# Kernel optimization log

Hardware: AMD Instinct MI355X
Metric: run time of the kernel (lower is better)

Reference implementation:

```python
import jax, jax.numpy as jnp
import numpy as np

N = 100000      # nodes
E = 1600000     # edges (avg degree 16)
IN = 128        # in_channels
H = 64          # hidden
C = 2           # num_classes
G = 256         # graphs in batch


def _glorot(key, shape):
    lim = np.sqrt(6.0 / (shape[0] + shape[1])).astype(np.float32)
    return jax.random.uniform(key, shape, jnp.float32, -lim, lim)


def setup_inputs() -> dict:
    key = jax.random.key(0)
    ks = jax.random.split(key, 8)
    x = jax.random.normal(ks[0], (N, IN), jnp.float32)
    edge_index = jax.random.randint(ks[1], (2, E), 0, N)
    batch = jnp.sort(jax.random.randint(ks[2], (N,), 0, G))
    W1 = _glorot(ks[3], (IN, H)); b1 = jnp.zeros((H,), jnp.float32)
    W2 = _glorot(ks[4], (H, H));  b2 = jnp.zeros((H,), jnp.float32)
    Wc1 = _glorot(ks[5], (H, H // 2)); bc1 = jnp.zeros((H // 2,), jnp.float32)
    Wc2 = _glorot(ks[6], (H // 2, C)); bc2 = jnp.zeros((C,), jnp.float32)
    return dict(x=x, edge_index=edge_index, batch=batch,
                W1=W1, b1=b1, W2=W2, b2=b2,
                Wc1=Wc1, bc1=bc1, Wc2=Wc2, bc2=bc2)


def gcn_conv(x, W, b, src, dst, n):
    """PyG GCNConv: linear -> symmetric-normalized scatter-add with self-loops."""
    h = x @ W                                   # [N, out]
    # degree over dst including the added self-loop (edge_weight = 1)
    deg = jax.ops.segment_sum(jnp.ones((src.shape[0],), h.dtype), dst,
                              num_segments=n) + 1.0
    dinv = jax.lax.rsqrt(deg)                   # deg^{-1/2}
    norm = dinv[src] * dinv[dst]                # [E]
    msg = norm[:, None] * h[src]                # gather + normalize
    out = jax.ops.segment_sum(msg, dst, num_segments=n)
    out = out + (dinv * dinv)[:, None] * h      # self-loop contribution
    return out + b


def reference(x, edge_index, batch, W1, b1, W2, b2, Wc1, bc1, Wc2, bc2):
    src, dst = edge_index[0], edge_index[1]
    h = jax.nn.relu(gcn_conv(x, W1, b1, src, dst, N))
    h = jax.nn.relu(gcn_conv(h, W2, b2, src, dst, N))
    # global mean pool over graph ids
    s = jax.ops.segment_sum(h, batch, num_segments=G)
    cnt = jax.ops.segment_sum(jnp.ones((N,), h.dtype), batch, num_segments=G)
    g = s / jnp.maximum(cnt, 1.0)[:, None]      # [G, H]
    return jax.nn.relu(g @ Wc1 + bc1) @ Wc2 + bc2  # [G, C]
```

## Files before the change

### kernel.cpp

```cpp
#include <hip/hip_runtime.h>

#define N_NODES 100000
#define N_EDGES 1600000
#define IN_CH   128
#define HID     64
#define NG      256
#define CAP     64
#define NXCD    8
#define XRANGE  ((N_NODES + NXCD - 1) / NXCD)

typedef __attribute__((ext_vector_type(8))) short bf16x8;
typedef __attribute__((ext_vector_type(4))) float f32x4;

__device__ __forceinline__ unsigned short f2bf(float f) {
    union { float f; unsigned u; } v; v.f = f;
    unsigned r = v.u + 0x7FFF + ((v.u >> 16) & 1);
    return (unsigned short)(r >> 16);
}
__device__ __forceinline__ float bfval(unsigned short h) {
    return __uint_as_float((unsigned)h << 16);
}
__device__ __forceinline__ unsigned int f2bf2(float lo, float hi) {
    return (unsigned int)f2bf(lo) | ((unsigned int)f2bf(hi) << 16);
}
__device__ __forceinline__ float bf_lo(unsigned int p) { return __uint_as_float(p << 16); }
__device__ __forceinline__ float bf_hi(unsigned int p) { return __uint_as_float(p & 0xFFFF0000u); }

__global__ void k_zero(int* __restrict__ p, int n4) {
    int i = blockIdx.x * blockDim.x + threadIdx.x;
    if (i < n4) reinterpret_cast<int4*>(p)[i] = (int4){0, 0, 0, 0};
}

__global__ void k_fillx(const int* __restrict__ src, const int* __restrict__ dst,
                        int* __restrict__ fillpos, int* __restrict__ col) {
    const int xcd = blockIdx.x & (NXCD - 1);
    const int chunk = blockIdx.x >> 3;
    const int nchunks = gridDim.x >> 3;
    const int lo = xcd * XRANGE;
    const int hi = (lo + XRANGE < N_NODES) ? lo + XRANGE : N_NODES;
    const int per = (N_EDGES + nchunks - 1) / nchunks;
    const int e0 = chunk * per;
    const int e1 = (e0 + per < N_EDGES) ? e0 + per : N_EDGES;
    for (int e = e0 + threadIdx.x; e < e1; e += blockDim.x) {
        int d = dst[e];
        if (d < lo || d >= hi) continue;
        int p = atomicAdd(&fillpos[d], 1);
        if (p < CAP) col[(long)d * CAP + p] = src[e];
    }
}

__global__ void k_prep(const int* __restrict__ deg, float* __restrict__ dinv,
                       int* __restrict__ col, const int* __restrict__ batch,
                       int* __restrict__ start) {
    int i = blockIdx.x * blockDim.x + threadIdx.x;
    if (i >= N_NODES) return;
    int n = deg[i];
    dinv[i] = rsqrtf((float)n + 1.0f);
    n = n < CAP ? n : CAP;
    int n16 = (n + 15) & ~15;
    int* crow = col + (long)i * CAP;
    for (int p = n; p < n16; ++p) crow[p] = i;
    int b = batch[i];
    int prev = (i == 0) ? -1 : batch[i - 1];
    for (int g = prev + 1; g <= b; ++g) start[g] = i;
    if (i == N_NODES - 1)
        for (int g = b + 1; g <= NG; ++g) start[g] = N_NODES;
}

__global__ void k_wcvt(const float* __restrict__ W1, const float* __restrict__ W2,
                       unsigned short* __restrict__ W1hi, unsigned short* __restrict__ W1lo,
                       unsigned short* __restrict__ W2hi, unsigned short* __restrict__ W2lo) {
    int t = blockIdx.x * blockDim.x + threadIdx.x;
    if (t < 64 * IN_CH) {
        int e = t & 7, lane = (t >> 3) & 63, q = t >> 9;
        int kk = q >> 2, cb = q & 3, kg = lane >> 4, r = lane & 15;
        float v = W1[(kk * 32 + kg * 8 + e) * 64 + cb * 16 + r];
        unsigned short hh = f2bf(v);
        W1hi[t] = hh;
        W1lo[t] = f2bf(v - bfval(hh));
    } else if (t < 64 * IN_CH + 64 * HID) {
        int t2 = t - 64 * IN_CH;
        int e = t2 & 7, lane = (t2 >> 3) & 63, q = t2 >> 9;
        int kk = q >> 2, cb = q & 3, kg = lane >> 4, r = lane & 15;
        float v = W2[(kk * 32 + kg * 8 + e) * 64 + cb * 16 + r];
        unsigned short hh = f2bf(v);
        W2hi[t2] = hh;
        W2lo[t2] = f2bf(v - bfval(hh));
    }
}

template <int K>
__global__ void __launch_bounds__(256) k_linear(const float* __restrict__ x,
                                                const unsigned short* __restrict__ Whi,
                                                const unsigned short* __restrict__ Wlo,
                                                const float* __restrict__ dinv,
                                                unsigned short* __restrict__ hs) {
    __shared__ f32x4 red[2][64][8];
    const int tid  = threadIdx.x;
    const int wv   = tid >> 6;
    const int pair = wv >> 1;
    const int h    = wv & 1;
    const int lane = tid & 63;
    const int row16 = lane & 15;
    const int kg    = lane >> 4;
    const int n0 = (blockIdx.x * 2 + pair) * 32;
    const bool valid = (n0 < N_NODES);

    f32x4 acc[2][4];
#pragma unroll
    for (int bt = 0; bt < 2; ++bt)
#pragma unroll
        for (int cb = 0; cb < 4; ++cb) acc[bt][cb] = (f32x4){0.f, 0.f, 0.f, 0.f};

    const int NKK = K / 32;
    const int kkBeg = h * (NKK / 2);
    const int kkEnd = kkBeg + NKK / 2;

#pragma unroll
    for (int kk = kkBeg; kk < kkEnd; ++kk) {
        bf16x8 xhi0, xlo0, xhi1, xlo1;
        {
            int rr = n0 + row16;
            rr = rr < N_NODES ? rr : N_NODES - 1;
            const float* ap = x + (long)rr * K + kk * 32 + kg * 8;
            float4 b0 = *reinterpret_cast<const float4*>(ap);
            float4 b1 = *reinterpret_cast<const float4*>(ap + 4);
#define CVT(dsthi, dstlo, i, val) { unsigned short h_ = f2bf(val); dsthi[i] = (short)h_; \
                                    dstlo[i] = (short)f2bf((val) - bfval(h_)); }
            CVT(xhi0, xlo0, 0, b0.x) CVT(xhi0, xlo0, 1, b0.y)
            CVT(xhi0, xlo0, 2, b0.z) CVT(xhi0, xlo0, 3, b0.w)
            CVT(xhi0, xlo0, 4, b1.x) CVT(xhi0, xlo0, 5, b1.y)
            CVT(xhi0, xlo0, 6, b1.z) CVT(xhi0, xlo0, 7, b1.w)
        }
        {
            int rr = n0 + 16 + row16;
            rr = rr < N_NODES ? rr : N_NODES - 1;
            const float* ap = x + (long)rr * K + kk * 32 + kg * 8;
            float4 b0 = *reinterpret_cast<const float4*>(ap);
            float4 b1 = *reinterpret_cast<const float4*>(ap + 4);
            CVT(xhi1, xlo1, 0, b0.x) CVT(xhi1, xlo1, 1, b0.y)
            CVT(xhi1, xlo1, 2, b0.z) CVT(xhi1, xlo1, 3, b0.w)
            CVT(xhi1, xlo1, 4, b1.x) CVT(xhi1, xlo1, 5, b1.y)
            CVT(xhi1, xlo1, 6, b1.z) CVT(xhi1, xlo1, 7, b1.w)
#undef CVT
        }
#pragma unroll
        for (int cb = 0; cb < 4; ++cb) {
            long foff = (long)((kk * 4 + cb) * 64 + lane) * 8;
            bf16x8 wh = *reinterpret_cast<const bf16x8*>(Whi + foff);
            bf16x8 wl = *reinterpret_cast<const bf16x8*>(Wlo + foff);
            acc[0][cb] = __builtin_amdgcn_mfma_f32_16x16x32_bf16(wh, xhi0, acc[0][cb], 0, 0, 0);
            acc[0][cb] = __builtin_amdgcn_mfma_f32_16x16x32_bf16(wh, xlo0, acc[0][cb], 0, 0, 0);
            acc[0][cb] = __builtin_amdgcn_mfma_f32_16x16x32_bf16(wl, xhi0, acc[0][cb], 0, 0, 0);
            acc[1][cb] = __builtin_amdgcn_mfma_f32_16x16x32_bf16(wh, xhi1, acc[1][cb], 0, 0, 0);
            acc[1][cb] = __builtin_amdgcn_mfma_f32_16x16x32_bf16(wh, xlo1, acc[1][cb], 0, 0, 0);
            acc[1][cb] = __builtin_amdgcn_mfma_f32_16x16x32_bf16(wl, xhi1, acc[1][cb], 0, 0, 0);
        }
    }

    if (h == 1) {
#pragma unroll
        for (int bt = 0; bt < 2; ++bt)
#pragma unroll
            for (int cb = 0; cb < 4; ++cb) red[pair][lane][bt * 4 + cb] = acc[bt][cb];
    }
    __syncthreads();
    if (h == 0 && valid) {
#pragma unroll
        for (int bt = 0; bt < 2; ++bt) {
            int n = n0 + bt * 16 + row16;
            float d = dinv[n];
#pragma unroll
            for (int cb = 0; cb < 4; ++cb) {
                f32x4 a = acc[bt][cb];
                f32x4 b = red[pair][lane][bt * 4 + cb];
                float v0 = (a[0] + b[0]) * d;
                float v1 = (a[1] + b[1]) * d;
                float v2 = (a[2] + b[2]) * d;
                float v3 = (a[3] + b[3]) * d;
                uint2 p;
                p.x = f2bf2(v0, v1);
                p.y = f2bf2(v2, v3);
                *reinterpret_cast<uint2*>(&hs[(long)n * 64 + cb * 16 + kg * 4]) = p;
            }
        }
    }
}

__global__ void k_gather(const int* __restrict__ deg, const int* __restrict__ col,
                         const unsigned int* __restrict__ hs2,
                         const float* __restrict__ dinv, const float* __restrict__ bias,
                         float* __restrict__ out) {
    int t = blockIdx.x * blockDim.x + threadIdx.x;
    int lane = t & 63;
    int half = lane >> 5;
    int c2 = lane & 31;
    int i = ((t >> 6) << 1) + half;
    if (i >= N_NODES) return;
    const int4* crow4 = reinterpret_cast<const int4*>(col + (long)i * CAP);
    int n = deg[i];
    n = n < CAP ? n : CAP;
    int n16 = (n + 15) & ~15;
    const unsigned int* hsc = hs2 + c2;
    unsigned int self = hsc[(long)i * 32];
    float selfL = bf_lo(self), selfH = bf_hi(self);
    float aL = selfL, aH = selfH;

    for (int e0 = 0; e0 < n16; e0 += 16) {
        int4 q0 = crow4[(e0 >> 2) + 0];
        int4 q1 = crow4[(e0 >> 2) + 1];
        int4 q2 = crow4[(e0 >> 2) + 2];
        int4 q3 = crow4[(e0 >> 2) + 3];
        unsigned int v[16];
        v[0]  = hsc[(long)q0.x * 32]; v[1]  = hsc[(long)q0.y * 32];
        v[2]  = hsc[(long)q0.z * 32]; v[3]  = hsc[(long)q0.w * 32];
        v[4]  = hsc[(long)q1.x * 32]; v[5]  = hsc[(long)q1.y * 32];
        v[6]  = hsc[(long)q1.z * 32]; v[7]  = hsc[(long)q1.w * 32];
        v[8]  = hsc[(long)q2.x * 32]; v[9]  = hsc[(long)q2.y * 32];
        v[10] = hsc[(long)q2.z * 32]; v[11] = hsc[(long)q2.w * 32];
        v[12] = hsc[(long)q3.x * 32]; v[13] = hsc[(long)q3.y * 32];
        v[14] = hsc[(long)q3.z * 32]; v[15] = hsc[(long)q3.w * 32];
#pragma unroll
        for (int j = 0; j < 16; ++j) {
            aL += bf_lo(v[j]);
            aH += bf_hi(v[j]);
        }
    }
    float fE = (float)(n16 - n);
    aL = fmaf(-fE, selfL, aL);
    aH = fmaf(-fE, selfH, aH);

    float di = dinv[i];
    float vL = fmaf(di, aL, bias[2 * c2]);
    float vH = fmaf(di, aH, bias[2 * c2 + 1]);
    float2 o;
    o.x = vL > 0.f ? vL : 0.f;
    o.y = vH > 0.f ? vH : 0.f;
    *reinterpret_cast<float2*>(&out[(long)i * 64 + 2 * c2]) = o;
}

__global__ void k_poolhead(const float* __restrict__ a, const int* __restrict__ start,
                           const float* __restrict__ Wc1, const float* __restrict__ bc1,
                           const float* __restrict__ Wc2, const float* __restrict__ bc2,
                           float* __restrict__ out) {
    __shared__ float partial[4][64];
    __shared__ float gvec[64];
    __shared__ float tvec[32];
    int g = blockIdx.x;
    int w = threadIdx.x >> 6;
    int j = threadIdx.x & 63;
    int s0 = start[g], s1 = start[g + 1];
    float acc = 0.f;
    for (int i = s0 + w; i < s1; i += 4)
        acc += a[(long)i * 64 + j];
    partial[w][j] = acc;
    __syncthreads();
    if (w == 0) {
        float c = (float)(s1 - s0);
        c = c > 1.f ? c : 1.f;
        gvec[j] = (partial[0][j] + partial[1][j] + partial[2][j] + partial[3][j]) / c;
    }
    __syncthreads();
    if (threadIdx.x < 32) {
        int jj = threadIdx.x;
        float acc2 = bc1[jj];
#pragma unroll 8
        for (int k = 0; k < 64; ++k) acc2 = fmaf(gvec[k], Wc1[k * 32 + jj], acc2);
        tvec[jj] = acc2 > 0.f ? acc2 : 0.f;
    }
    __syncthreads();
    if (threadIdx.x < 2) {
        int jj = threadIdx.x;
        float acc2 = bc2[jj];
#pragma unroll
        for (int k = 0; k < 32; ++k) acc2 = fmaf(tvec[k], Wc2[k * 2 + jj], acc2);
        out[g * 2 + jj] = acc2;
    }
}

extern "C" void kernel_launch(void* const* d_in, const int* in_sizes, int n_in,
                              void* d_out, int out_size, void* d_ws, size_t ws_size,
                              hipStream_t stream) {
    const float* x    = (const float*)d_in[0];
    const int*   ei   = (const int*)d_in[1];
    const int*   batch= (const int*)d_in[2];
    const float* W1   = (const float*)d_in[3];
    const float* b1   = (const float*)d_in[4];
    const float* W2   = (const float*)d_in[5];
    const float* b2   = (const float*)d_in[6];
    const float* Wc1  = (const float*)d_in[7];
    const float* bc1  = (const float*)d_in[8];
    const float* Wc2  = (const float*)d_in[9];
    const float* bc2  = (const float*)d_in[10];
    float* out = (float*)d_out;

    const int* src = ei;
    const int* dst = ei + N_EDGES;

    char* ws = (char*)d_ws;
    size_t off = 0;
    auto alloc = [&](size_t bytes) {
        void* p = ws + off;
        off += (bytes + 255) & ~(size_t)255;
        return p;
    };
    unsigned short* hs = (unsigned short*)alloc((size_t)N_NODES * HID * 2);
    float* agg     = (float*)alloc((size_t)N_NODES * HID * sizeof(float));
    int*   col     = (int*)  alloc((size_t)N_NODES * CAP * sizeof(int) + 256);
    float* dinv    = (float*)alloc(N_NODES * sizeof(float));
    int*   fillpos = (int*)  alloc((N_NODES + 4) * sizeof(int));
    int*   start   = (int*)  alloc((NG + 1) * sizeof(int));
    unsigned short* W1hi = (unsigned short*)alloc(64 * IN_CH * 2);
    unsigned short* W1lo = (unsigned short*)alloc(64 * IN_CH * 2);
    unsigned short* W2hi = (unsigned short*)alloc(64 * HID * 2);
    unsigned short* W2lo = (unsigned short*)alloc(64 * HID * 2);

    const int TB = 256;

    k_wcvt<<<(64 * (IN_CH + HID) + TB - 1) / TB, TB, 0, stream>>>(W1, W2, W1hi, W1lo, W2hi, W2lo);

    {
        const int nz4 = (N_NODES + 3) / 4;
        k_zero<<<(nz4 + TB - 1) / TB, TB, 0, stream>>>(fillpos, nz4);
        k_fillx<<<2048, TB, 0, stream>>>(src, dst, fillpos, col);
        k_prep<<<(N_NODES + TB - 1) / TB, TB, 0, stream>>>(fillpos, dinv, col, batch, start);
    }

    const int gatherBlocks = ((N_NODES + 1) / 2 * 64 + TB - 1) / TB;
    const int linBlocks = (N_NODES + 63) / 64;

    k_linear<IN_CH><<<linBlocks, 256, 0, stream>>>(x, W1hi, W1lo, dinv, hs);
    k_gather<<<gatherBlocks, TB, 0, stream>>>(fillpos, col, (const unsigned int*)hs, dinv, b1, agg);

    k_linear<HID><<<linBlocks, 256, 0, stream>>>(agg, W2hi, W2lo, dinv, hs);
    k_gather<<<gatherBlocks, TB, 0, stream>>>(fillpos, col, (const unsigned int*)hs, dinv, b2, agg);

    k_poolhead<<<NG, 256, 0, stream>>>(agg, start, Wc1, bc1, Wc2, bc2, out);
}
```

Baseline: 212.9 us.

## Co-schedule first linear layer with CSR fill in one fused launch

```diff
diff --git a/kernel.cpp b/kernel.cpp
--- a/kernel.cpp
+++ b/kernel.cpp
@@ -8,6 +8,8 @@
 #define CAP     64
 #define NXCD    8
 #define XRANGE  ((N_NODES + NXCD - 1) / NXCD)
+#define FILLB   2048
+#define LINB    ((N_NODES + 63) / 64)
 
 typedef __attribute__((ext_vector_type(8))) short bf16x8;
 typedef __attribute__((ext_vector_type(4))) float f32x4;
@@ -26,51 +28,12 @@
 __device__ __forceinline__ float bf_lo(unsigned int p) { return __uint_as_float(p << 16); }
 __device__ __forceinline__ float bf_hi(unsigned int p) { return __uint_as_float(p & 0xFFFF0000u); }
 
-__global__ void k_zero(int* __restrict__ p, int n4) {
-    int i = blockIdx.x * blockDim.x + threadIdx.x;
-    if (i < n4) reinterpret_cast<int4*>(p)[i] = (int4){0, 0, 0, 0};
-}
-
-__global__ void k_fillx(const int* __restrict__ src, const int* __restrict__ dst,
-                        int* __restrict__ fillpos, int* __restrict__ col) {
-    const int xcd = blockIdx.x & (NXCD - 1);
-    const int chunk = blockIdx.x >> 3;
-    const int nchunks = gridDim.x >> 3;
-    const int lo = xcd * XRANGE;
-    const int hi = (lo + XRANGE < N_NODES) ? lo + XRANGE : N_NODES;
-    const int per = (N_EDGES + nchunks - 1) / nchunks;
-    const int e0 = chunk * per;
-    const int e1 = (e0 + per < N_EDGES) ? e0 + per : N_EDGES;
-    for (int e = e0 + threadIdx.x; e < e1; e += blockDim.x) {
-        int d = dst[e];
-        if (d < lo || d >= hi) continue;
-        int p = atomicAdd(&fillpos[d], 1);
-        if (p < CAP) col[(long)d * CAP + p] = src[e];
-    }
-}
-
-__global__ void k_prep(const int* __restrict__ deg, float* __restrict__ dinv,
-                       int* __restrict__ col, const int* __restrict__ batch,
-                       int* __restrict__ start) {
-    int i = blockIdx.x * blockDim.x + threadIdx.x;
-    if (i >= N_NODES) return;
-    int n = deg[i];
-    dinv[i] = rsqrtf((float)n + 1.0f);
-    n = n < CAP ? n : CAP;
-    int n16 = (n + 15) & ~15;
-    int* crow = col + (long)i * CAP;
-    for (int p = n; p < n16; ++p) crow[p] = i;
-    int b = batch[i];
-    int prev = (i == 0) ? -1 : batch[i - 1];
-    for (int g = prev + 1; g <= b; ++g) start[g] = i;
-    if (i == N_NODES - 1)
-        for (int g = b + 1; g <= NG; ++g) start[g] = N_NODES;
-}
-
-__global__ void k_wcvt(const float* __restrict__ W1, const float* __restrict__ W2,
+__global__ void k_init(const float* __restrict__ W1, const float* __restrict__ W2,
                        unsigned short* __restrict__ W1hi, unsigned short* __restrict__ W1lo,
-                       unsigned short* __restrict__ W2hi, unsigned short* __restrict__ W2lo) {
+                       unsigned short* __restrict__ W2hi, unsigned short* __restrict__ W2lo,
+                       int* __restrict__ fillpos) {
     int t = blockIdx.x * blockDim.x + threadIdx.x;
+    if (t < N_NODES / 4) reinterpret_cast<int4*>(fillpos)[t] = (int4){0, 0, 0, 0};
     if (t < 64 * IN_CH) {
         int e = t & 7, lane = (t >> 3) & 63, q = t >> 9;
         int kk = q >> 2, cb = q & 3, kg = lane >> 4, r = lane & 15;
@@ -89,21 +52,18 @@
     }
 }
 
-template <int K>
-__global__ void __launch_bounds__(256) k_linear(const float* __restrict__ x,
-                                                const unsigned short* __restrict__ Whi,
-                                                const unsigned short* __restrict__ Wlo,
-                                                const float* __restrict__ dinv,
-                                                unsigned short* __restrict__ hs) {
-    __shared__ f32x4 red[2][64][8];
-    const int tid  = threadIdx.x;
+template <int K, bool SC>
+__device__ __forceinline__ void lin_body(int bid, int tid, const float* __restrict__ x,
+        const unsigned short* __restrict__ Whi, const unsigned short* __restrict__ Wlo,
+        const float* __restrict__ dinv, unsigned short* __restrict__ hs,
+        float* __restrict__ fout, f32x4 red[2][64][8]) {
     const int wv   = tid >> 6;
     const int pair = wv >> 1;
     const int h    = wv & 1;
     const int lane = tid & 63;
     const int row16 = lane & 15;
     const int kg    = lane >> 4;
-    const int n0 = (blockIdx.x * 2 + pair) * 32;
+    const int n0 = (bid * 2 + pair) * 32;
     const bool valid = (n0 < N_NODES);
 
     f32x4 acc[2][4];
@@ -169,25 +129,92 @@
 #pragma unroll
         for (int bt = 0; bt < 2; ++bt) {
             int n = n0 + bt * 16 + row16;
-            float d = dinv[n];
 #pragma unroll
             for (int cb = 0; cb < 4; ++cb) {
                 f32x4 a = acc[bt][cb];
                 f32x4 b = red[pair][lane][bt * 4 + cb];
-                float v0 = (a[0] + b[0]) * d;
-                float v1 = (a[1] + b[1]) * d;
-                float v2 = (a[2] + b[2]) * d;
-                float v3 = (a[3] + b[3]) * d;
-                uint2 p;
-                p.x = f2bf2(v0, v1);
-                p.y = f2bf2(v2, v3);
-                *reinterpret_cast<uint2*>(&hs[(long)n * 64 + cb * 16 + kg * 4]) = p;
+                if (SC) {
+                    float d = dinv[n];
+                    uint2 p;
+                    p.x = f2bf2((a[0] + b[0]) * d, (a[1] + b[1]) * d);
+                    p.y = f2bf2((a[2] + b[2]) * d, (a[3] + b[3]) * d);
+                    *reinterpret_cast<uint2*>(&hs[(long)n * 64 + cb * 16 + kg * 4]) = p;
+                } else {
+                    float4 st;
+                    st.x = a[0] + b[0]; st.y = a[1] + b[1];
+                    st.z = a[2] + b[2]; st.w = a[3] + b[3];
+                    *reinterpret_cast<float4*>(&fout[(long)n * 64 + cb * 16 + kg * 4]) = st;
+                }
             }
         }
     }
 }
 
-__global__ void k_gather(const int* __restrict__ deg, const int* __restrict__ col,
+__global__ void __launch_bounds__(256) k_fuse(const float* __restrict__ x,
+        const unsigned short* __restrict__ W1hi, const unsigned short* __restrict__ W1lo,
+        float* __restrict__ agg,
+        const int* __restrict__ src, const int* __restrict__ dst,
+        int* __restrict__ fillpos, int* __restrict__ col) {
+    __shared__ f32x4 red[2][64][8];
+    if (blockIdx.x < LINB) {
+        lin_body<IN_CH, false>(blockIdx.x, threadIdx.x, x, W1hi, W1lo, nullptr, nullptr, agg, red);
+    } else {
+        const int fb = blockIdx.x - LINB;
+        const int xcd = fb & (NXCD - 1);
+        const int chunk = fb >> 3;
+        const int nchunks = FILLB >> 3;
+        const int lo = xcd * XRANGE;
+        const int hi = (lo + XRANGE < N_NODES) ? lo + XRANGE : N_NODES;
+        const int per = (N_EDGES + nchunks - 1) / nchunks;
+        const int e0 = chunk * per;
+        const int e1 = (e0 + per < N_EDGES) ? e0 + per : N_EDGES;
+        for (int e = e0 + threadIdx.x; e < e1; e += blockDim.x) {
+            int d = dst[e];
+            if (d < lo || d >= hi) continue;
+            int p = atomicAdd(&fillpos[d], 1);
+            if (p < CAP) col[(long)d * CAP + p] = src[e] * 32;
+        }
+    }
+}
+
+template <int K>
+__global__ void __launch_bounds__(256) k_linear(const float* __restrict__ x,
+        const unsigned short* __restrict__ Whi, const unsigned short* __restrict__ Wlo,
+        const float* __restrict__ dinv, unsigned short* __restrict__ hs) {
+    __shared__ f32x4 red[2][64][8];
+    lin_body<K, true>(blockIdx.x, threadIdx.x, x, Whi, Wlo, dinv, hs, nullptr, red);
+}
+
+__global__ void k_prep(const int* __restrict__ fillpos, float* __restrict__ dinv,
+                       int* __restrict__ col, const int* __restrict__ batch,
+                       int* __restrict__ start) {
+    int i = blockIdx.x * blockDim.x + threadIdx.x;
+    if (i >= N_NODES) return;
+    int n = fillpos[i];
+    dinv[i] = rsqrtf((float)n + 1.0f);
+    n = n < CAP ? n : CAP;
+    int n16 = (n + 15) & ~15;
+    int* crow = col + (long)i * CAP;
+    int self32 = i * 32;
+    for (int p = n; p < n16; ++p) crow[p] = self32;
+    int b = batch[i];
+    int prev = (i == 0) ? -1 : batch[i - 1];
+    for (int g = prev + 1; g <= b; ++g) start[g] = i;
+    if (i == N_NODES - 1)
+        for (int g = b + 1; g <= NG; ++g) start[g] = N_NODES;
+}
+
+__global__ void k_scale(const float* __restrict__ fin, const float* __restrict__ dinv,
+                        unsigned int* __restrict__ hs2) {
+    int t = blockIdx.x * blockDim.x + threadIdx.x;
+    if (t >= N_NODES * 32) return;
+    int n = t >> 5;
+    float d = dinv[n];
+    float2 a = reinterpret_cast<const float2*>(fin)[t];
+    hs2[t] = f2bf2(a.x * d, a.y * d);
+}
+
+__global__ void k_gather(const int* __restrict__ fillpos, const int* __restrict__ col,
                          const unsigned int* __restrict__ hs2,
                          const float* __restrict__ dinv, const float* __restrict__ bias,
                          float* __restrict__ out) {
@@ -198,7 +225,7 @@
     int i = ((t >> 6) << 1) + half;
     if (i >= N_NODES) return;
     const int4* crow4 = reinterpret_cast<const int4*>(col + (long)i * CAP);
-    int n = deg[i];
+    int n = fillpos[i];
     n = n < CAP ? n : CAP;
     int n16 = (n + 15) & ~15;
     const unsigned int* hsc = hs2 + c2;
@@ -212,14 +239,14 @@
         int4 q2 = crow4[(e0 >> 2) + 2];
         int4 q3 = crow4[(e0 >> 2) + 3];
         unsigned int v[16];
-        v[0]  = hsc[(long)q0.x * 32]; v[1]  = hsc[(long)q0.y * 32];
-        v[2]  = hsc[(long)q0.z * 32]; v[3]  = hsc[(long)q0.w * 32];
-        v[4]  = hsc[(long)q1.x * 32]; v[5]  = hsc[(long)q1.y * 32];
-        v[6]  = hsc[(long)q1.z * 32]; v[7]  = hsc[(long)q1.w * 32];
-        v[8]  = hsc[(long)q2.x * 32]; v[9]  = hsc[(long)q2.y * 32];
-        v[10] = hsc[(long)q2.z * 32]; v[11] = hsc[(long)q2.w * 32];
-        v[12] = hsc[(long)q3.x * 32]; v[13] = hsc[(long)q3.y * 32];
-        v[14] = hsc[(long)q3.z * 32]; v[15] = hsc[(long)q3.w * 32];
+        v[0]  = hsc[(long)q0.x]; v[1]  = hsc[(long)q0.y];
+        v[2]  = hsc[(long)q0.z]; v[3]  = hsc[(long)q0.w];
+        v[4]  = hsc[(long)q1.x]; v[5]  = hsc[(long)q1.y];
+        v[6]  = hsc[(long)q1.z]; v[7]  = hsc[(long)q1.w];
+        v[8]  = hsc[(long)q2.x]; v[9]  = hsc[(long)q2.y];
+        v[10] = hsc[(long)q2.z]; v[11] = hsc[(long)q2.w];
+        v[12] = hsc[(long)q3.x]; v[13] = hsc[(long)q3.y];
+        v[14] = hsc[(long)q3.z]; v[15] = hsc[(long)q3.w];
 #pragma unroll
         for (int j = 0; j < 16; ++j) {
             aL += bf_lo(v[j]);
@@ -317,22 +344,19 @@
 
     const int TB = 256;
 
-    k_wcvt<<<(64 * (IN_CH + HID) + TB - 1) / TB, TB, 0, stream>>>(W1, W2, W1hi, W1lo, W2hi, W2lo);
-
-    {
-        const int nz4 = (N_NODES + 3) / 4;
-        k_zero<<<(nz4 + TB - 1) / TB, TB, 0, stream>>>(fillpos, nz4);
-        k_fillx<<<2048, TB, 0, stream>>>(src, dst, fillpos, col);
-        k_prep<<<(N_NODES + TB - 1) / TB, TB, 0, stream>>>(fillpos, dinv, col, batch, start);
-    }
+    k_init<<<(N_NODES / 4 + TB - 1) / TB, TB, 0, stream>>>(W1, W2, W1hi, W1lo, W2hi, W2lo, fillpos);
+
+    k_fuse<<<LINB + FILLB, TB, 0, stream>>>(x, W1hi, W1lo, agg, src, dst, fillpos, col);
+
+    k_prep<<<(N_NODES + TB - 1) / TB, TB, 0, stream>>>(fillpos, dinv, col, batch, start);
+
+    k_scale<<<(N_NODES * 32 + TB - 1) / TB, TB, 0, stream>>>(agg, dinv, (unsigned int*)hs);
 
     const int gatherBlocks = ((N_NODES + 1) / 2 * 64 + TB - 1) / TB;
-    const int linBlocks = (N_NODES + 63) / 64;
-
-    k_linear<IN_CH><<<linBlocks, 256, 0, stream>>>(x, W1hi, W1lo, dinv, hs);
+
     k_gather<<<gatherBlocks, TB, 0, stream>>>(fillpos, col, (const unsigned int*)hs, dinv, b1, agg);
 
-    k_linear<HID><<<linBlocks, 256, 0, stream>>>(agg, W2hi, W2lo, dinv, hs);
+    k_linear<HID><<<LINB, TB, 0, stream>>>(agg, W2hi, W2lo, dinv, hs);
     k_gather<<<gatherBlocks, TB, 0, stream>>>(fillpos, col, (const unsigned int*)hs, dinv, b2, agg);
 
     k_poolhead<<<NG, 256, 0, stream>>>(agg, start, Wc1, bc1, Wc2, bc2, out);
```

New measurement: 214.7 us. About the same (+0.8%).

## Build CSR with LDS-local counting and two-pass placement instead of global atomics

Applied to the files above, without the earlier changes.

```diff
diff --git a/kernel.cpp b/kernel.cpp
--- a/kernel.cpp
+++ b/kernel.cpp
@@ -7,7 +7,10 @@
 #define NG      256
 #define CAP     64
 #define NXCD    8
-#define XRANGE  ((N_NODES + NXCD - 1) / NXCD)
+#define XRANGE  (N_NODES / NXCD)
+#define NSLICE  32
+#define PERSLICE (N_EDGES / NSLICE)
+#define LINB    ((N_NODES + 63) / 64)
 
 typedef __attribute__((ext_vector_type(8))) short bf16x8;
 typedef __attribute__((ext_vector_type(4))) float f32x4;
@@ -25,47 +28,6 @@
 }
 __device__ __forceinline__ float bf_lo(unsigned int p) { return __uint_as_float(p << 16); }
 __device__ __forceinline__ float bf_hi(unsigned int p) { return __uint_as_float(p & 0xFFFF0000u); }
-
-__global__ void k_zero(int* __restrict__ p, int n4) {
-    int i = blockIdx.x * blockDim.x + threadIdx.x;
-    if (i < n4) reinterpret_cast<int4*>(p)[i] = (int4){0, 0, 0, 0};
-}
-
-__global__ void k_fillx(const int* __restrict__ src, const int* __restrict__ dst,
-                        int* __restrict__ fillpos, int* __restrict__ col) {
-    const int xcd = blockIdx.x & (NXCD - 1);
-    const int chunk = blockIdx.x >> 3;
-    const int nchunks = gridDim.x >> 3;
-    const int lo = xcd * XRANGE;
-    const int hi = (lo + XRANGE < N_NODES) ? lo + XRANGE : N_NODES;
-    const int per = (N_EDGES + nchunks - 1) / nchunks;
-    const int e0 = chunk * per;
-    const int e1 = (e0 + per < N_EDGES) ? e0 + per : N_EDGES;
-    for (int e = e0 + threadIdx.x; e < e1; e += blockDim.x) {
-        int d = dst[e];
-        if (d < lo || d >= hi) continue;
-        int p = atomicAdd(&fillpos[d], 1);
-        if (p < CAP) col[(long)d * CAP + p] = src[e];
-    }
-}
-
-__global__ void k_prep(const int* __restrict__ deg, float* __restrict__ dinv,
-                       int* __restrict__ col, const int* __restrict__ batch,
-                       int* __restrict__ start) {
-    int i = blockIdx.x * blockDim.x + threadIdx.x;
-    if (i >= N_NODES) return;
-    int n = deg[i];
-    dinv[i] = rsqrtf((float)n + 1.0f);
-    n = n < CAP ? n : CAP;
-    int n16 = (n + 15) & ~15;
-    int* crow = col + (long)i * CAP;
-    for (int p = n; p < n16; ++p) crow[p] = i;
-    int b = batch[i];
-    int prev = (i == 0) ? -1 : batch[i - 1];
-    for (int g = prev + 1; g <= b; ++g) start[g] = i;
-    if (i == N_NODES - 1)
-        for (int g = b + 1; g <= NG; ++g) start[g] = N_NODES;
-}
 
 __global__ void k_wcvt(const float* __restrict__ W1, const float* __restrict__ W2,
                        unsigned short* __restrict__ W1hi, unsigned short* __restrict__ W1lo,
@@ -89,6 +51,95 @@
     }
 }
 
+__global__ void __launch_bounds__(1024) k_cntA(const int* __restrict__ dst,
+                                               int* __restrict__ cnt32) {
+    __shared__ int c[XRANGE];
+    const int r = blockIdx.x & (NXCD - 1);
+    const int s = blockIdx.x >> 3;
+    const int lo = r * XRANGE;
+    for (int j = threadIdx.x; j < XRANGE; j += 1024) c[j] = 0;
+    __syncthreads();
+    const int4* d4 = reinterpret_cast<const int4*>(dst + s * PERSLICE);
+    for (int q = threadIdx.x; q < PERSLICE / 4; q += 1024) {
+        int4 v = d4[q];
+        int t;
+        t = v.x - lo; if ((unsigned)t < XRANGE) atomicAdd(&c[t], 1);
+        t = v.y - lo; if ((unsigned)t < XRANGE) atomicAdd(&c[t], 1);
+        t = v.z - lo; if ((unsigned)t < XRANGE) atomicAdd(&c[t], 1);
+        t = v.w - lo; if ((unsigned)t < XRANGE) atomicAdd(&c[t], 1);
+    }
+    __syncthreads();
+    int* outp = cnt32 + (long)s * N_NODES + lo;
+    for (int j = threadIdx.x; j < XRANGE; j += 1024) outp[j] = c[j];
+}
+
+__global__ void k_prep(int* __restrict__ cnt32, int* __restrict__ deg,
+                       float* __restrict__ dinv, int* __restrict__ col,
+                       const int* __restrict__ batch, int* __restrict__ start) {
+    int i = blockIdx.x * blockDim.x + threadIdx.x;
+    if (i >= N_NODES) return;
+    int run = 0;
+#pragma unroll
+    for (int s = 0; s < NSLICE; ++s) {
+        long idx = (long)s * N_NODES + i;
+        int v = cnt32[idx];
+        cnt32[idx] = run;
+        run += v;
+    }
+    deg[i] = run;
+    dinv[i] = rsqrtf((float)run + 1.0f);
+    int n = run < CAP ? run : CAP;
+    int n16 = (n + 15) & ~15;
+    int* crow = col + (long)i * CAP;
+    int self32 = i * 32;
+    for (int p = n; p < n16; ++p) crow[p] = self32;
+    int b = batch[i];
+    int prev = (i == 0) ? -1 : batch[i - 1];
+    for (int g = prev + 1; g <= b; ++g) start[g] = i;
+    if (i == N_NODES - 1)
+        for (int g = b + 1; g <= NG; ++g) start[g] = N_NODES;
+}
+
+__global__ void __launch_bounds__(1024) k_place(const int* __restrict__ src,
+                                                const int* __restrict__ dst,
+                                                const int* __restrict__ off32,
+                                                int* __restrict__ col) {
+    __shared__ int c[XRANGE];
+    const int r = blockIdx.x & (NXCD - 1);
+    const int s = blockIdx.x >> 3;
+    const int lo = r * XRANGE;
+    for (int j = threadIdx.x; j < XRANGE; j += 1024) c[j] = 0;
+    __syncthreads();
+    const int4* d4 = reinterpret_cast<const int4*>(dst + s * PERSLICE);
+    const int4* s4 = reinterpret_cast<const int4*>(src + s * PERSLICE);
+    const int* obase = off32 + (long)s * N_NODES;
+    for (int q = threadIdx.x; q < PERSLICE / 4; q += 1024) {
+        int4 v = d4[q];
+        int4 u = s4[q];
+        int t, p;
+        t = v.x - lo;
+        if ((unsigned)t < XRANGE) {
+            p = atomicAdd(&c[t], 1) + obase[v.x];
+            if (p < CAP) col[(long)v.x * CAP + p] = u.x * 32;
+        }
+        t = v.y - lo;
+        if ((unsigned)t < XRANGE) {
+            p = atomicAdd(&c[t], 1) + obase[v.y];
+            if (p < CAP) col[(long)v.y * CAP + p] = u.y * 32;
+        }
+        t = v.z - lo;
+        if ((unsigned)t < XRANGE) {
+            p = atomicAdd(&c[t], 1) + obase[v.z];
+            if (p < CAP) col[(long)v.z * CAP + p] = u.z * 32;
+        }
+        t = v.w - lo;
+        if ((unsigned)t < XRANGE) {
+            p = atomicAdd(&c[t], 1) + obase[v.w];
+            if (p < CAP) col[(long)v.w * CAP + p] = u.w * 32;
+        }
+    }
+}
+
 template <int K>
 __global__ void __launch_bounds__(256) k_linear(const float* __restrict__ x,
                                                 const unsigned short* __restrict__ Whi,
@@ -174,13 +225,9 @@
             for (int cb = 0; cb < 4; ++cb) {
                 f32x4 a = acc[bt][cb];
                 f32x4 b = red[pair][lane][bt * 4 + cb];
-                float v0 = (a[0] + b[0]) * d;
-                float v1 = (a[1] + b[1]) * d;
-                float v2 = (a[2] + b[2]) * d;
-                float v3 = (a[3] + b[3]) * d;
                 uint2 p;
-                p.x = f2bf2(v0, v1);
-                p.y = f2bf2(v2, v3);
+                p.x = f2bf2((a[0] + b[0]) * d, (a[1] + b[1]) * d);
+                p.y = f2bf2((a[2] + b[2]) * d, (a[3] + b[3]) * d);
                 *reinterpret_cast<uint2*>(&hs[(long)n * 64 + cb * 16 + kg * 4]) = p;
             }
         }
@@ -212,14 +259,14 @@
         int4 q2 = crow4[(e0 >> 2) + 2];
         int4 q3 = crow4[(e0 >> 2) + 3];
         unsigned int v[16];
-        v[0]  = hsc[(long)q0.x * 32]; v[1]  = hsc[(long)q0.y * 32];
-        v[2]  = hsc[(long)q0.z * 32]; v[3]  = hsc[(long)q0.w * 32];
-        v[4]  = hsc[(long)q1.x * 32]; v[5]  = hsc[(long)q1.y * 32];
-        v[6]  = hsc[(long)q1.z * 32]; v[7]  = hsc[(long)q1.w * 32];
-        v[8]  = hsc[(long)q2.x * 32]; v[9]  = hsc[(long)q2.y * 32];
-        v[10] = hsc[(long)q2.z * 32]; v[11] = hsc[(long)q2.w * 32];
-        v[12] = hsc[(long)q3.x * 32]; v[13] = hsc[(long)q3.y * 32];
-        v[14] = hsc[(long)q3.z * 32]; v[15] = hsc[(long)q3.w * 32];
+        v[0]  = hsc[(long)q0.x]; v[1]  = hsc[(long)q0.y];
+        v[2]  = hsc[(long)q0.z]; v[3]  = hsc[(long)q0.w];
+        v[4]  = hsc[(long)q1.x]; v[5]  = hsc[(long)q1.y];
+        v[6]  = hsc[(long)q1.z]; v[7]  = hsc[(long)q1.w];
+        v[8]  = hsc[(long)q2.x]; v[9]  = hsc[(long)q2.y];
+        v[10] = hsc[(long)q2.z]; v[11] = hsc[(long)q2.w];
+        v[12] = hsc[(long)q3.x]; v[13] = hsc[(long)q3.y];
+        v[14] = hsc[(long)q3.z]; v[15] = hsc[(long)q3.w];
 #pragma unroll
         for (int j = 0; j < 16; ++j) {
             aL += bf_lo(v[j]);
@@ -307,8 +354,9 @@
     unsigned short* hs = (unsigned short*)alloc((size_t)N_NODES * HID * 2);
     float* agg     = (float*)alloc((size_t)N_NODES * HID * sizeof(float));
     int*   col     = (int*)  alloc((size_t)N_NODES * CAP * sizeof(int) + 256);
+    int*   cnt32   = (int*)  alloc((size_t)NSLICE * N_NODES * sizeof(int));
     float* dinv    = (float*)alloc(N_NODES * sizeof(float));
-    int*   fillpos = (int*)  alloc((N_NODES + 4) * sizeof(int));
+    int*   deg     = (int*)  alloc(N_NODES * sizeof(int));
     int*   start   = (int*)  alloc((NG + 1) * sizeof(int));
     unsigned short* W1hi = (unsigned short*)alloc(64 * IN_CH * 2);
     unsigned short* W1lo = (unsigned short*)alloc(64 * IN_CH * 2);
@@ -319,21 +367,17 @@
 
     k_wcvt<<<(64 * (IN_CH + HID) + TB - 1) / TB, TB, 0, stream>>>(W1, W2, W1hi, W1lo, W2hi, W2lo);
 
-    {
-        const int nz4 = (N_NODES + 3) / 4;
-        k_zero<<<(nz4 + TB - 1) / TB, TB, 0, stream>>>(fillpos, nz4);
-        k_fillx<<<2048, TB, 0, stream>>>(src, dst, fillpos, col);
-        k_prep<<<(N_NODES + TB - 1) / TB, TB, 0, stream>>>(fillpos, dinv, col, batch, start);
-    }
+    k_cntA<<<NXCD * NSLICE, 1024, 0, stream>>>(dst, cnt32);
+    k_prep<<<(N_NODES + TB - 1) / TB, TB, 0, stream>>>(cnt32, deg, dinv, col, batch, start);
+    k_place<<<NXCD * NSLICE, 1024, 0, stream>>>(src, dst, cnt32, col);
 
     const int gatherBlocks = ((N_NODES + 1) / 2 * 64 + TB - 1) / TB;
-    const int linBlocks = (N_NODES + 63) / 64;
-
-    k_linear<IN_CH><<<linBlocks, 256, 0, stream>>>(x, W1hi, W1lo, dinv, hs);
-    k_gather<<<gatherBlocks, TB, 0, stream>>>(fillpos, col, (const unsigned int*)hs, dinv, b1, agg);
-
-    k_linear<HID><<<linBlocks, 256, 0, stream>>>(agg, W2hi, W2lo, dinv, hs);
-    k_gather<<<gatherBlocks, TB, 0, stream>>>(fillpos, col, (const unsigned int*)hs, dinv, b2, agg);
+
+    k_linear<IN_CH><<<LINB, TB, 0, stream>>>(x, W1hi, W1lo, dinv, hs);
+    k_gather<<<gatherBlocks, TB, 0, stream>>>(deg, col, (const unsigned int*)hs, dinv, b1, agg);
+
+    k_linear<HID><<<LINB, TB, 0, stream>>>(agg, W2hi, W2lo, dinv, hs);
+    k_gather<<<gatherBlocks, TB, 0, stream>>>(deg, col, (const unsigned int*)hs, dinv, b2, agg);
 
     k_poolhead<<<NG, 256, 0, stream>>>(agg, start, Wc1, bc1, Wc2, bc2, out);
 }
```

Result: faster. 194.6 us (-8.6%).
